# Optimization experiments

Hardware: AMD Instinct MI355X
Metric: run time of the kernel (lower is better)

## Reference

```python
import jax, jax.numpy as jnp
import numpy as np

N, C, B = 800000, 64, 8
BN_EPS = 1e-5


def setup_inputs() -> dict:
    key = jax.random.key(0)
    ks = jax.random.split(key, 8)
    x = jax.random.normal(ks[0], (N, C), dtype=jnp.float32)
    # cumulative end-offsets of B equal segments: [100000, 200000, ..., 800000]
    o = (jnp.arange(1, B + 1, dtype=jnp.int64) * (N // B))
    s2 = 1.0 / np.sqrt(C)
    s1 = 1.0 / np.sqrt(2 * C)
    w2 = jax.random.uniform(ks[1], (C, C), jnp.float32, -s2, s2)      # linear2 Linear(C,C)
    b2 = jax.random.uniform(ks[2], (C,), jnp.float32, -s2, s2)
    w1 = jax.random.uniform(ks[3], (C, 2 * C), jnp.float32, -s1, s1)  # linear1 Linear(2C,C)
    b1 = jax.random.uniform(ks[4], (C,), jnp.float32, -s1, s1)
    gamma = jnp.ones((C,), jnp.float32)   # BatchNorm1d weight
    beta = jnp.zeros((C,), jnp.float32)   # BatchNorm1d bias
    return {"x": x, "o": o, "w2": w2, "b2": b2, "w1": w1, "b1": b1,
            "gamma": gamma, "beta": beta}


def reference(x, o, w2, b2, w1, b1, gamma, beta):
    n = x.shape[0]
    nb = o.shape[0]
    # segment id of each point: point i belongs to segment j iff o[j-1] <= i < o[j]
    seg = jnp.searchsorted(o, jnp.arange(n), side="right")          # [N]
    counts = jnp.diff(o, prepend=0).astype(x.dtype)                  # [B]
    # per-segment mean pool
    means = jax.ops.segment_sum(x, seg, num_segments=nb) / counts[:, None]  # [B, C]
    # linear2: Linear + ReLU on pooled vectors
    h = jax.nn.relu(means @ w2.T + b2)                               # [B, C]
    # broadcast pooled features back to points and concat
    cat = jnp.concatenate([x, h[seg]], axis=1)                       # [N, 2C]
    # linear1: Linear + BatchNorm1d (training-mode batch stats) + ReLU
    y = cat @ w1.T + b1                                              # [N, C]
    mu = y.mean(axis=0)
    var = y.var(axis=0)
    y = (y - mu) * jax.lax.rsqrt(var + BN_EPS) * gamma + beta
    return jax.nn.relu(y)
```

## Files before the change

### kernel.cpp

```cpp
#include <hip/hip_runtime.h>

#define NROWS 800000
#define SEGROWS 100000
#define K1_BLOCKS 800
#define K1_ROWS 1000

typedef __attribute__((ext_vector_type(8))) short bf16x8;
typedef __attribute__((ext_vector_type(4))) float f32x4;
typedef __attribute__((ext_vector_type(4))) short short4v;

__device__ inline unsigned short f2bf(float f) {
    unsigned u = __builtin_bit_cast(unsigned, f);
    return (unsigned short)((u + 0x7FFFu + ((u >> 16) & 1u)) >> 16);
}

__global__ void kzero(float* __restrict__ p) {
    int t = blockIdx.x * 256 + threadIdx.x;
    if (t < 4608) p[t] = 0.f;
}

__global__ __launch_bounds__(256, 2)
void k1_stats(const float* __restrict__ x, float* __restrict__ m2g, float* __restrict__ ssumg)
{
    __shared__ __align__(16) float smem[5120];
    short* xt = (short*)smem;
    const float4* X4 = (const float4*)x;
    int t = threadIdx.x, w = t >> 6, lane = t & 63;
    int c4 = t & 15, g = t >> 4;
    size_t r0 = (size_t)blockIdx.x * K1_ROWS;
    int seg = (int)(r0 / SEGROWS);

    f32x4 acc[4][4];
#pragma unroll
    for (int p = 0; p < 4; ++p)
#pragma unroll
        for (int q = 0; q < 4; ++q) acc[p][q] = (f32x4){0.f, 0.f, 0.f, 0.f};
    float s0 = 0, s1 = 0, s2 = 0, s3 = 0;

    for (int tile = 0; tile < K1_ROWS; tile += 128) {
        int nr = min(128, K1_ROWS - tile);
        __syncthreads();
#pragma unroll
        for (int h = 0; h < 2; ++h) {
            int rg = 8 * g + 4 * h;
            float4 v[4];
#pragma unroll
            for (int i = 0; i < 4; ++i) {
                int r = rg + i;
                if (r < nr) {
                    v[i] = X4[(r0 + tile + r) * 16 + c4];
                    s0 += v[i].x; s1 += v[i].y; s2 += v[i].z; s3 += v[i].w;
                } else v[i] = make_float4(0.f, 0.f, 0.f, 0.f);
            }
#pragma unroll
            for (int j = 0; j < 4; ++j) {
                short4v pk;
                pk[0] = (short)f2bf(((const float*)&v[0])[j]);
                pk[1] = (short)f2bf(((const float*)&v[1])[j]);
                pk[2] = (short)f2bf(((const float*)&v[2])[j]);
                pk[3] = (short)f2bf(((const float*)&v[3])[j]);
                *(short4v*)&xt[(4 * c4 + j) * 136 + rg] = pk;
            }
        }
        __syncthreads();
        bf16x8 f[4];
#pragma unroll
        for (int c0 = 0; c0 < 4; ++c0)
            f[c0] = *(const bf16x8*)&xt[(16 * c0 + (lane & 15)) * 136 + 32 * w + 8 * (lane >> 4)];
#pragma unroll
        for (int p = 0; p < 4; ++p)
#pragma unroll
            for (int q = 0; q < 4; ++q)
                acc[p][q] = __builtin_amdgcn_mfma_f32_16x16x32_bf16(f[p], f[q], acc[p][q], 0, 0, 0);
    }

    __syncthreads();
    ((float4*)(smem + 4096))[t] = make_float4(s0, s1, s2, s3);
    int qd = lane >> 4, cl = lane & 15;
    if (w == 0) {
#pragma unroll
        for (int p = 0; p < 4; ++p)
#pragma unroll
            for (int q = 0; q < 4; ++q)
#pragma unroll
                for (int i = 0; i < 4; ++i)
                    smem[(16 * p + 4 * qd + i) * 64 + 16 * q + cl] = acc[p][q][i];
    }
    __syncthreads();
    if (t < 64) {
        int cc4 = t >> 2, ii = t & 3;
        float s = 0;
#pragma unroll
        for (int u = 0; u < 16; ++u) s += smem[4096 + 4 * (cc4 + 16 * u) + ii];
        atomicAdd(&ssumg[seg * 64 + t], s);
    }
    for (int ww = 1; ww < 4; ++ww) {
        if (w == ww) {
#pragma unroll
            for (int p = 0; p < 4; ++p)
#pragma unroll
                for (int q = 0; q < 4; ++q)
#pragma unroll
                    for (int i = 0; i < 4; ++i)
                        smem[(16 * p + 4 * qd + i) * 64 + 16 * q + cl] += acc[p][q][i];
        }
        __syncthreads();
    }
    for (int f2 = t; f2 < 4096; f2 += 256) atomicAdd(&m2g[f2], smem[f2]);
}

__global__ __launch_bounds__(256)
void k2b_solve(const int* __restrict__ o,
               const float* __restrict__ w2, const float* __restrict__ b2,
               const float* __restrict__ w1, const float* __restrict__ b1,
               const float* __restrict__ gamma, const float* __restrict__ beta,
               const float* __restrict__ m2, const float* __restrict__ ssum,
               unsigned short* __restrict__ wpb, float* __restrict__ tbout)
{
    __shared__ __align__(16) float w1s[8192];
    __shared__ __align__(16) float w2s[4096];
    __shared__ __align__(16) float m2s[4096];
    __shared__ __align__(16) float ssums[512];
    __shared__ float means[512], hb[512], cv[512], q1p[256];
    __shared__ float Sx[64], muS[64], sS[64], cnts[8];

    int t = threadIdx.x;
    for (int i = t; i < 2048; i += 256) ((float4*)w1s)[i] = ((const float4*)w1)[i];
    for (int i = t; i < 1024; i += 256) ((float4*)w2s)[i] = ((const float4*)w2)[i];
    for (int i = t; i < 1024; i += 256) ((float4*)m2s)[i] = ((const float4*)m2)[i];
    for (int i = t; i < 128;  i += 256) ((float4*)ssums)[i] = ((const float4*)ssum)[i];
    if (t < 8) cnts[t] = (float)(o[t] - (t ? o[t - 1] : 0));
    __syncthreads();

    for (int i = t; i < 512; i += 256) means[i] = ssums[i] / cnts[i >> 6];
    __syncthreads();
    int c = t & 63, g = t >> 6;
    for (int b = g; b < 8; b += 4) {
        float a = b2[c];
        for (int k = 0; k < 64; ++k) a = fmaf(means[b * 64 + k], w2s[c * 64 + k], a);
        hb[b * 64 + c] = fmaxf(a, 0.f);
    }
    __syncthreads();
    for (int b = g; b < 8; b += 4) {
        float a = b1[c];
        for (int k = 0; k < 64; ++k) a = fmaf(hb[b * 64 + k], w1s[c * 128 + 64 + k], a);
        cv[b * 64 + c] = a;
    }
    __syncthreads();
    if (t < 64) {
        float s = 0;
        for (int b = 0; b < 8; ++b) s += ssums[b * 64 + t];
        Sx[t] = s;
    }
    __syncthreads();
    {
        float p = 0;
        for (int j = g * 16; j < g * 16 + 16; ++j) {
            float vj = 0;
            for (int k = 0; k < 64; ++k) vj = fmaf(w1s[c * 128 + k], m2s[j * 64 + k], vj);
            p = fmaf(w1s[c * 128 + j], vj, p);
        }
        q1p[g * 64 + c] = p;
    }
    __syncthreads();
    if (t < 64) {
        const float Nf = (float)NROWS;
        float mu = 0;
        for (int k = 0; k < 64; ++k) mu = fmaf(w1s[t * 128 + k], Sx[k], mu);
        float q2 = 0, q3 = 0, msum = 0;
        for (int b = 0; b < 8; ++b) {
            float gv = cv[b * 64 + t];
            msum += cnts[b] * gv;
            q3 = fmaf(cnts[b] * gv, gv, q3);
            float dot = 0;
            for (int k = 0; k < 64; ++k) dot = fmaf(w1s[t * 128 + k], ssums[b * 64 + k], dot);
            q2 = fmaf(2.f * gv, dot, q2);
        }
        mu = (mu + msum) / Nf;
        float q1 = q1p[t] + q1p[64 + t] + q1p[128 + t] + q1p[192 + t];
        float var = (q1 + q2 + q3) / Nf - mu * mu;
        float s = gamma[t] * rsqrtf(var + 1e-5f);
        muS[t] = mu; sS[t] = s;
    }
    __syncthreads();
    for (int f = t; f < 4096; f += 256)
        wpb[f] = f2bf(w1s[(f >> 6) * 128 + (f & 63)] * sS[f >> 6]);
    for (int f = t; f < 512; f += 256)
        tbout[f] = (cv[f] - muS[f & 63]) * sS[f & 63] + beta[f & 63];
}

__global__ __launch_bounds__(256, 3)
void k3_gemm(const float* __restrict__ x, const unsigned short* __restrict__ wpb,
             const float* __restrict__ tb, float* __restrict__ out)
{
    __shared__ __align__(16) short bt[64 * 72];
    __shared__ float tbs[512];
    int t = threadIdx.x, lane = t & 63, w = t >> 6;
    size_t r0 = (size_t)blockIdx.x * 256;

    for (int f = t; f < 512; f += 256) {
        int c = f >> 3, kg = f & 7;
        uint4 vv = ((const uint4*)wpb)[f];
        *(uint4*)&bt[c * 72 + kg * 8] = vv;
    }
    for (int f = t; f < 512; f += 256) tbs[f] = tb[f];
    __syncthreads();

    int cl = lane & 15, qd = lane >> 4;
    bf16x8 B[4][2];
#pragma unroll
    for (int n = 0; n < 4; ++n)
#pragma unroll
        for (int k0 = 0; k0 < 2; ++k0)
            B[n][k0] = *(const bf16x8*)&bt[(16 * n + cl) * 72 + 32 * k0 + 8 * qd];

    int rbase = (int)r0 + 64 * w;
    f32x4 acc[4][4];
#pragma unroll
    for (int m = 0; m < 4; ++m)
#pragma unroll
        for (int n = 0; n < 4; ++n) acc[m][n] = (f32x4){0.f, 0.f, 0.f, 0.f};

#pragma unroll
    for (int m = 0; m < 4; ++m) {
        const float* rp = x + (size_t)(rbase + 16 * m + cl) * 64 + 8 * qd;
        float4 u0 = *(const float4*)(rp);
        float4 u1 = *(const float4*)(rp + 4);
        float4 u2 = *(const float4*)(rp + 32);
        float4 u3 = *(const float4*)(rp + 36);
        bf16x8 A0, A1;
        A0[0] = (short)f2bf(u0.x); A0[1] = (short)f2bf(u0.y);
        A0[2] = (short)f2bf(u0.z); A0[3] = (short)f2bf(u0.w);
        A0[4] = (short)f2bf(u1.x); A0[5] = (short)f2bf(u1.y);
        A0[6] = (short)f2bf(u1.z); A0[7] = (short)f2bf(u1.w);
        A1[0] = (short)f2bf(u2.x); A1[1] = (short)f2bf(u2.y);
        A1[2] = (short)f2bf(u2.z); A1[3] = (short)f2bf(u2.w);
        A1[4] = (short)f2bf(u3.x); A1[5] = (short)f2bf(u3.y);
        A1[6] = (short)f2bf(u3.z); A1[7] = (short)f2bf(u3.w);
#pragma unroll
        for (int n = 0; n < 4; ++n) {
            acc[m][n] = __builtin_amdgcn_mfma_f32_16x16x32_bf16(A0, B[n][0], acc[m][n], 0, 0, 0);
            acc[m][n] = __builtin_amdgcn_mfma_f32_16x16x32_bf16(A1, B[n][1], acc[m][n], 0, 0, 0);
        }
    }

    int seg0 = rbase / SEGROWS;
    int bnd = (seg0 + 1) * SEGROWS;
    int seg1 = min(seg0 + 1, 7);
    float tA[4], tB[4];
#pragma unroll
    for (int n = 0; n < 4; ++n) {
        tA[n] = tbs[seg0 * 64 + 16 * n + cl];
        tB[n] = tbs[seg1 * 64 + 16 * n + cl];
    }
#pragma unroll
    for (int m = 0; m < 4; ++m)
#pragma unroll
        for (int i = 0; i < 4; ++i) {
            int grow = rbase + 16 * m + 4 * qd + i;
            bool hi = grow >= bnd;
#pragma unroll
            for (int n = 0; n < 4; ++n) {
                float tv = hi ? tB[n] : tA[n];
                float vv = fmaxf(acc[m][n][i] + tv, 0.f);
                out[(size_t)grow * 64 + 16 * n + cl] = vv;
            }
        }
}

extern "C" void kernel_launch(void* const* d_in, const int* in_sizes, int n_in,
                              void* d_out, int out_size, void* d_ws, size_t ws_size,
                              hipStream_t stream)
{
    const float* x  = (const float*)d_in[0];
    const int*   o  = (const int*)d_in[1];
    const float* w2 = (const float*)d_in[2];
    const float* b2 = (const float*)d_in[3];
    const float* w1 = (const float*)d_in[4];
    const float* b1 = (const float*)d_in[5];
    const float* gm = (const float*)d_in[6];
    const float* bt = (const float*)d_in[7];
    float* out = (float*)d_out;
    float* ws  = (float*)d_ws;

    float*          m2g  = ws;
    float*          ssum = ws + 4096;
    float*          tbv  = ws + 4608;
    unsigned short* wpb  = (unsigned short*)(ws + 5120);

    kzero<<<18, 256, 0, stream>>>(ws);
    k1_stats<<<K1_BLOCKS, 256, 0, stream>>>(x, m2g, ssum);
    k2b_solve<<<1, 256, 0, stream>>>(o, w2, b2, w1, b1, gm, bt, m2g, ssum, wpb, tbv);
    k3_gemm<<<3125, 256, 0, stream>>>(x, wpb, tbv, out);
}
```

Measured before the change: 443.8 us.

## Spread Gram-matrix atomics over per-segment copies and batch global loads

The Gram-matrix atomic accumulation in the stats kernel now targets eight per-segment partial copies, with rotated start offsets per block, so the 800 blocks no longer all contend on one 4096-float buffer. The solve kernel sums the eight partials itself. The stats kernel gets a fast path for full 128-row tiles that issues eight loads before packing to bf16. The GEMM kernel hoists all x loads ahead of the B fragment reads and lowers its occupancy hint to 2 to make room for the extra registers. Costs are a larger zeroing pass, more reads in the single-block solve kernel, and possibly lower occupancy in the GEMM kernel.

```diff
diff --git a/kernel.cpp b/kernel.cpp
--- a/kernel.cpp
+++ b/kernel.cpp
@@ -16,11 +16,11 @@
 
 __global__ void kzero(float* __restrict__ p) {
     int t = blockIdx.x * 256 + threadIdx.x;
-    if (t < 4608) p[t] = 0.f;
+    if (t < 33280) p[t] = 0.f;
 }
 
 __global__ __launch_bounds__(256, 2)
-void k1_stats(const float* __restrict__ x, float* __restrict__ m2g, float* __restrict__ ssumg)
+void k1_stats(const float* __restrict__ x, float* __restrict__ m2p, float* __restrict__ ssumg)
 {
     __shared__ __align__(16) float smem[5120];
     short* xt = (short*)smem;
@@ -40,26 +40,45 @@
     for (int tile = 0; tile < K1_ROWS; tile += 128) {
         int nr = min(128, K1_ROWS - tile);
         __syncthreads();
-#pragma unroll
-        for (int h = 0; h < 2; ++h) {
-            int rg = 8 * g + 4 * h;
-            float4 v[4];
-#pragma unroll
-            for (int i = 0; i < 4; ++i) {
-                int r = rg + i;
-                if (r < nr) {
-                    v[i] = X4[(r0 + tile + r) * 16 + c4];
-                    s0 += v[i].x; s1 += v[i].y; s2 += v[i].z; s3 += v[i].w;
-                } else v[i] = make_float4(0.f, 0.f, 0.f, 0.f);
+        if (nr == 128) {
+            float4 v[8];
+#pragma unroll
+            for (int i = 0; i < 8; ++i)
+                v[i] = X4[(r0 + tile + 8 * g + i) * 16 + c4];
+#pragma unroll
+            for (int i = 0; i < 8; ++i) {
+                s0 += v[i].x; s1 += v[i].y; s2 += v[i].z; s3 += v[i].w;
             }
 #pragma unroll
             for (int j = 0; j < 4; ++j) {
-                short4v pk;
-                pk[0] = (short)f2bf(((const float*)&v[0])[j]);
-                pk[1] = (short)f2bf(((const float*)&v[1])[j]);
-                pk[2] = (short)f2bf(((const float*)&v[2])[j]);
-                pk[3] = (short)f2bf(((const float*)&v[3])[j]);
-                *(short4v*)&xt[(4 * c4 + j) * 136 + rg] = pk;
+                bf16x8 pk;
+#pragma unroll
+                for (int i = 0; i < 8; ++i)
+                    pk[i] = (short)f2bf(((const float*)&v[i])[j]);
+                *(bf16x8*)&xt[(4 * c4 + j) * 136 + 8 * g] = pk;
+            }
+        } else {
+#pragma unroll
+            for (int h = 0; h < 2; ++h) {
+                int rg = 8 * g + 4 * h;
+                float4 v[4];
+#pragma unroll
+                for (int i = 0; i < 4; ++i) {
+                    int r = rg + i;
+                    if (r < nr) {
+                        v[i] = X4[(r0 + tile + r) * 16 + c4];
+                        s0 += v[i].x; s1 += v[i].y; s2 += v[i].z; s3 += v[i].w;
+                    } else v[i] = make_float4(0.f, 0.f, 0.f, 0.f);
+                }
+#pragma unroll
+                for (int j = 0; j < 4; ++j) {
+                    short4v pk;
+                    pk[0] = (short)f2bf(((const float*)&v[0])[j]);
+                    pk[1] = (short)f2bf(((const float*)&v[1])[j]);
+                    pk[2] = (short)f2bf(((const float*)&v[2])[j]);
+                    pk[3] = (short)f2bf(((const float*)&v[3])[j]);
+                    *(short4v*)&xt[(4 * c4 + j) * 136 + rg] = pk;
+                }
             }
         }
         __syncthreads();
@@ -106,7 +125,12 @@
         }
         __syncthreads();
     }
-    for (int f2 = t; f2 < 4096; f2 += 256) atomicAdd(&m2g[f2], smem[f2]);
+    float* m2seg = m2p + seg * 4096;
+#pragma unroll
+    for (int ii = 0; ii < 16; ++ii) {
+        int f2 = t + 256 * ((ii + blockIdx.x) & 15);
+        atomicAdd(&m2seg[f2], smem[f2]);
+    }
 }
 
 __global__ __launch_bounds__(256)
@@ -114,7 +138,7 @@
                const float* __restrict__ w2, const float* __restrict__ b2,
                const float* __restrict__ w1, const float* __restrict__ b1,
                const float* __restrict__ gamma, const float* __restrict__ beta,
-               const float* __restrict__ m2, const float* __restrict__ ssum,
+               const float* __restrict__ m2p, const float* __restrict__ ssum,
                unsigned short* __restrict__ wpb, float* __restrict__ tbout)
 {
     __shared__ __align__(16) float w1s[8192];
@@ -127,7 +151,15 @@
     int t = threadIdx.x;
     for (int i = t; i < 2048; i += 256) ((float4*)w1s)[i] = ((const float4*)w1)[i];
     for (int i = t; i < 1024; i += 256) ((float4*)w2s)[i] = ((const float4*)w2)[i];
-    for (int i = t; i < 1024; i += 256) ((float4*)m2s)[i] = ((const float4*)m2)[i];
+    for (int i = t; i < 1024; i += 256) {
+        float4 a = ((const float4*)m2p)[i];
+#pragma unroll
+        for (int s = 1; s < 8; ++s) {
+            float4 b = ((const float4*)m2p)[s * 1024 + i];
+            a.x += b.x; a.y += b.y; a.z += b.z; a.w += b.w;
+        }
+        ((float4*)m2s)[i] = a;
+    }
     for (int i = t; i < 128;  i += 256) ((float4*)ssums)[i] = ((const float4*)ssum)[i];
     if (t < 8) cnts[t] = (float)(o[t] - (t ? o[t - 1] : 0));
     __syncthreads();
@@ -189,7 +221,7 @@
         tbout[f] = (cv[f] - muS[f & 63]) * sS[f & 63] + beta[f & 63];
 }
 
-__global__ __launch_bounds__(256, 3)
+__global__ __launch_bounds__(256, 2)
 void k3_gemm(const float* __restrict__ x, const unsigned short* __restrict__ wpb,
              const float* __restrict__ tb, float* __restrict__ out)
 {
@@ -207,6 +239,18 @@
     __syncthreads();
 
     int cl = lane & 15, qd = lane >> 4;
+    int rbase = (int)r0 + 64 * w;
+
+    float4 u[4][4];
+#pragma unroll
+    for (int m = 0; m < 4; ++m) {
+        const float* rp = x + (size_t)(rbase + 16 * m + cl) * 64 + 8 * qd;
+        u[m][0] = *(const float4*)(rp);
+        u[m][1] = *(const float4*)(rp + 4);
+        u[m][2] = *(const float4*)(rp + 32);
+        u[m][3] = *(const float4*)(rp + 36);
+    }
+
     bf16x8 B[4][2];
 #pragma unroll
     for (int n = 0; n < 4; ++n)
@@ -214,7 +258,6 @@
         for (int k0 = 0; k0 < 2; ++k0)
             B[n][k0] = *(const bf16x8*)&bt[(16 * n + cl) * 72 + 32 * k0 + 8 * qd];
 
-    int rbase = (int)r0 + 64 * w;
     f32x4 acc[4][4];
 #pragma unroll
     for (int m = 0; m < 4; ++m)
@@ -223,20 +266,15 @@
 
 #pragma unroll
     for (int m = 0; m < 4; ++m) {
-        const float* rp = x + (size_t)(rbase + 16 * m + cl) * 64 + 8 * qd;
-        float4 u0 = *(const float4*)(rp);
-        float4 u1 = *(const float4*)(rp + 4);
-        float4 u2 = *(const float4*)(rp + 32);
-        float4 u3 = *(const float4*)(rp + 36);
         bf16x8 A0, A1;
-        A0[0] = (short)f2bf(u0.x); A0[1] = (short)f2bf(u0.y);
-        A0[2] = (short)f2bf(u0.z); A0[3] = (short)f2bf(u0.w);
-        A0[4] = (short)f2bf(u1.x); A0[5] = (short)f2bf(u1.y);
-        A0[6] = (short)f2bf(u1.z); A0[7] = (short)f2bf(u1.w);
-        A1[0] = (short)f2bf(u2.x); A1[1] = (short)f2bf(u2.y);
-        A1[2] = (short)f2bf(u2.z); A1[3] = (short)f2bf(u2.w);
-        A1[4] = (short)f2bf(u3.x); A1[5] = (short)f2bf(u3.y);
-        A1[6] = (short)f2bf(u3.z); A1[7] = (short)f2bf(u3.w);
+        A0[0] = (short)f2bf(u[m][0].x); A0[1] = (short)f2bf(u[m][0].y);
+        A0[2] = (short)f2bf(u[m][0].z); A0[3] = (short)f2bf(u[m][0].w);
+        A0[4] = (short)f2bf(u[m][1].x); A0[5] = (short)f2bf(u[m][1].y);
+        A0[6] = (short)f2bf(u[m][1].z); A0[7] = (short)f2bf(u[m][1].w);
+        A1[0] = (short)f2bf(u[m][2].x); A1[1] = (short)f2bf(u[m][2].y);
+        A1[2] = (short)f2bf(u[m][2].z); A1[3] = (short)f2bf(u[m][2].w);
+        A1[4] = (short)f2bf(u[m][3].x); A1[5] = (short)f2bf(u[m][3].y);
+        A1[6] = (short)f2bf(u[m][3].z); A1[7] = (short)f2bf(u[m][3].w);
 #pragma unroll
         for (int n = 0; n < 4; ++n) {
             acc[m][n] = __builtin_amdgcn_mfma_f32_16x16x32_bf16(A0, B[n][0], acc[m][n], 0, 0, 0);
@@ -283,13 +321,13 @@
     float* out = (float*)d_out;
     float* ws  = (float*)d_ws;
 
-    float*          m2g  = ws;
-    float*          ssum = ws + 4096;
-    float*          tbv  = ws + 4608;
-    unsigned short* wpb  = (unsigned short*)(ws + 5120);
-
-    kzero<<<18, 256, 0, stream>>>(ws);
-    k1_stats<<<K1_BLOCKS, 256, 0, stream>>>(x, m2g, ssum);
-    k2b_solve<<<1, 256, 0, stream>>>(o, w2, b2, w1, b1, gm, bt, m2g, ssum, wpb, tbv);
+    float*          m2p  = ws;
+    float*          ssum = ws + 32768;
+    float*          tbv  = ws + 33280;
+    unsigned short* wpb  = (unsigned short*)(ws + 33792);
+
+    kzero<<<130, 256, 0, stream>>>(ws);
+    k1_stats<<<K1_BLOCKS, 256, 0, stream>>>(x, m2p, ssum);
+    k2b_solve<<<1, 256, 0, stream>>>(o, w2, b2, w1, b1, gm, bt, m2p, ssum, wpb, tbv);
     k3_gemm<<<3125, 256, 0, stream>>>(x, wpb, tbv, out);
 }
```

Result: faster. 434.1 us (-2.2%).
